# Kernel optimization log

Hardware: AMD Instinct MI355X
Metric: run time of the kernel (lower is better)

## Reference

```python
import jax, jax.numpy as jnp
import numpy as np

N = 100000
E = 640000
D = 128


def _sage_conv(x, src, dst, Wp, bp, Wl, bl, Wr):
    # project=True: project + relu source features before aggregation
    h = jax.nn.relu(x @ Wp.T + bp)            # [N, D]
    msgs = h[src]                              # [E, D] gather
    summed = jax.ops.segment_sum(msgs, dst, num_segments=N)   # [N, D]
    cnt = jax.ops.segment_sum(jnp.ones((msgs.shape[0],), x.dtype), dst, num_segments=N)
    mean = summed / jnp.maximum(cnt, 1.0)[:, None]
    # lin_l on aggregated neighbors (with bias) + lin_r on root (no bias)
    return mean @ Wl.T + bl + x @ Wr.T


def setup_inputs() -> dict:
    key = jax.random.key(0)
    ks = jax.random.split(key, 16)
    s = 1.0 / np.sqrt(D)
    x = jax.random.normal(ks[0], (N, D), dtype=jnp.float32)
    edge_index = jax.random.randint(ks[1], (2, E), 0, N, dtype=jnp.int64)
    params = {}
    for i, base in enumerate(["conv0", "conv1"]):
        params[base + "_Wp"] = jax.random.uniform(ks[2 + 5 * i], (D, D), jnp.float32, -s, s)
        params[base + "_bp"] = jax.random.uniform(ks[3 + 5 * i], (D,), jnp.float32, -s, s)
        params[base + "_Wl"] = jax.random.uniform(ks[4 + 5 * i], (D, D), jnp.float32, -s, s)
        params[base + "_bl"] = jax.random.uniform(ks[5 + 5 * i], (D,), jnp.float32, -s, s)
        params[base + "_Wr"] = jax.random.uniform(ks[6 + 5 * i], (D, D), jnp.float32, -s, s)
    return {"x": x, "edge_index": edge_index, **params}


def reference(x, edge_index,
              conv0_Wp, conv0_bp, conv0_Wl, conv0_bl, conv0_Wr,
              conv1_Wp, conv1_bp, conv1_Wl, conv1_bl, conv1_Wr):
    src, dst = edge_index[0], edge_index[1]
    h = _sage_conv(x, src, dst, conv0_Wp, conv0_bp, conv0_Wl, conv0_bl, conv0_Wr)
    h = jax.nn.relu(h)
    return _sage_conv(h, src, dst, conv1_Wp, conv1_bp, conv1_Wl, conv1_bl, conv1_Wr)
```

## Files before the change

kernel.cpp:

```cpp
#include <hip/hip_runtime.h>

#define DD 128

typedef _Float16 f16;
typedef __attribute__((ext_vector_type(8))) _Float16 v8h;
typedef __attribute__((ext_vector_type(4))) _Float16 v4h;
typedef __attribute__((ext_vector_type(4))) float f32x4;

static inline int cdiv(int a, int b) { return (a + b - 1) / b; }


__global__ __launch_bounds__(256) void zero_kernel(int* __restrict__ p, int n) {
    int i = blockIdx.x * 256 + threadIdx.x;
    if (i < n) p[i] = 0;
}


__global__ __launch_bounds__(256) void count_kernel(const int* __restrict__ dst, int E,
                                                    int* __restrict__ cnt) {
    int e = blockIdx.x * 256 + threadIdx.x;
    if (e < E) atomicAdd(&cnt[dst[e]], 1);
}

__global__ __launch_bounds__(256) void scan1(const int* __restrict__ cnt, int N,
                                             int* __restrict__ bsum) {
    __shared__ int s[256];
    int i = blockIdx.x * 256 + threadIdx.x;
    s[threadIdx.x] = (i < N) ? cnt[i] : 0;
    __syncthreads();
    for (int off = 128; off > 0; off >>= 1) {
        if (threadIdx.x < off) s[threadIdx.x] += s[threadIdx.x + off];
        __syncthreads();
    }
    if (threadIdx.x == 0) bsum[blockIdx.x] = s[0];
}

__global__ __launch_bounds__(512) void scan2(const int* __restrict__ bsum, int NB,
                                             int* __restrict__ boff) {
    __shared__ int s[512];
    int t = threadIdx.x;
    int v = (t < NB) ? bsum[t] : 0;
    s[t] = v;
    __syncthreads();
    for (int off = 1; off < 512; off <<= 1) {
        int x = (t >= off) ? s[t - off] : 0;
        __syncthreads();
        s[t] += x;
        __syncthreads();
    }
    if (t < NB) boff[t] = s[t] - v;
}

__global__ __launch_bounds__(256) void scan3(const int* __restrict__ cnt,
                                             const int* __restrict__ boff, int N,
                                             int* __restrict__ off) {
    __shared__ int s[256];
    int t = threadIdx.x;
    int i = blockIdx.x * 256 + t;
    int v = (i < N) ? cnt[i] : 0;
    s[t] = v;
    __syncthreads();
    for (int o = 1; o < 256; o <<= 1) {
        int x = (t >= o) ? s[t - o] : 0;
        __syncthreads();
        s[t] += x;
        __syncthreads();
    }
    int excl = s[t] - v + boff[blockIdx.x];
    if (i < N) off[i] = excl;
    if (i == N - 1) off[N] = excl + v;
}

__global__ __launch_bounds__(256) void fill_kernel(const int* __restrict__ src,
                                                   const int* __restrict__ dst, int E,
                                                   const int* __restrict__ off,
                                                   int* __restrict__ cnt,
                                                   int* __restrict__ csr) {
    int e = blockIdx.x * 256 + threadIdx.x;
    if (e < E) {
        int d = dst[e];
        int p = atomicSub(&cnt[d], 1) - 1;
        csr[off[d] + p] = src[e];
    }
}


__global__ __launch_bounds__(256) void cvt_w_kernel(const float* __restrict__ W0,
                                                    const float* __restrict__ W1,
                                                    const float* __restrict__ W2,
                                                    const float* __restrict__ W3,
                                                    const float* __restrict__ W4,
                                                    const float* __restrict__ W5,
                                                    f16* __restrict__ out) {
    int mat = blockIdx.x >> 4;
    const float* W = mat == 0 ? W0 : mat == 1 ? W1 : mat == 2 ? W2
                   : mat == 3 ? W3 : mat == 4 ? W4 : W5;
    int base = (blockIdx.x & 15) * 1024 + threadIdx.x * 4;
    float4 v = *(const float4*)(W + base);
    v4h o;
    o[0] = (f16)v.x; o[1] = (f16)v.y; o[2] = (f16)v.z; o[3] = (f16)v.w;
    *(v4h*)(out + mat * 16384 + base) = o;
}


__device__ inline void stage_w(const f16* __restrict__ Wg, f16* __restrict__ smem, int t) {
#pragma unroll
    for (int i = 0; i < 8; ++i) {
        int idx16 = i * 256 + t;
        int col = idx16 >> 4, c16 = idx16 & 15;
        int sc = c16 ^ (col & 7);
        uint4 v = *(const uint4*)(Wg + idx16 * 8);
        *(uint4*)(smem + col * DD + sc * 8) = v;
    }
}

__device__ inline v8h read_b(const f16* __restrict__ smem, int ct, int ki, int l) {
    int col = ct * 16 + (l & 15);
    int c16 = ki * 4 + (l >> 4);
    int sc = c16 ^ (col & 7);
    return *(const v8h*)(smem + col * DD + sc * 8);
}

__device__ inline v8h load_frag16(const f16* __restrict__ A, int row, int kb, int M) {
    if (row >= M) {
        v8h z = {};
        return z;
    }
    return *(const v8h*)(A + (size_t)row * DD + kb);
}


template <typename TA, bool WX>
__global__ __launch_bounds__(256) void mgemm(const TA* __restrict__ A,
                                             const f16* __restrict__ W1,
                                             const float* __restrict__ bias,
                                             f16* __restrict__ OUT,
                                             f16* __restrict__ A16, int M) {
    __shared__ f16 WS[DD * DD];
    int t = threadIdx.x, l = t & 63, w = t >> 6;
    int row0 = blockIdx.x * 128 + w * 32;
    int r = l & 15, cg = l >> 4;

    stage_w(W1, WS, t);

    v8h af[2][4];
#pragma unroll
    for (int rt = 0; rt < 2; ++rt) {
        int row = row0 + rt * 16 + r;
#pragma unroll
        for (int ki = 0; ki < 4; ++ki) {
            int kb = ki * 32 + cg * 8;
            if constexpr (sizeof(TA) == 2) {
                af[rt][ki] = load_frag16(A, row, kb, M);
            } else {
                if (row < M) {
                    float4 a = *(const float4*)(A + (size_t)row * DD + kb);
                    float4 b = *(const float4*)(A + (size_t)row * DD + kb + 4);
                    v8h rr;
                    rr[0] = (f16)a.x; rr[1] = (f16)a.y; rr[2] = (f16)a.z; rr[3] = (f16)a.w;
                    rr[4] = (f16)b.x; rr[5] = (f16)b.y; rr[6] = (f16)b.z; rr[7] = (f16)b.w;
                    af[rt][ki] = rr;
                } else {
                    v8h z = {};
                    af[rt][ki] = z;
                }
            }
            if constexpr (WX) {
                if (row < M) *(v8h*)(A16 + (size_t)row * DD + kb) = af[rt][ki];
            }
        }
    }
    __syncthreads();

    f32x4 acc[2][8];
#pragma unroll
    for (int ct = 0; ct < 8; ++ct) {
        float bv = bias[ct * 16 + r];
        f32x4 b4 = {bv, bv, bv, bv};
        acc[0][ct] = b4;
        acc[1][ct] = b4;
    }

#pragma unroll
    for (int ct = 0; ct < 8; ++ct)
#pragma unroll
        for (int ki = 0; ki < 4; ++ki) {
            v8h b = read_b(WS, ct, ki, l);
            acc[0][ct] = __builtin_amdgcn_mfma_f32_16x16x32_f16(af[0][ki], b, acc[0][ct], 0, 0, 0);
            acc[1][ct] = __builtin_amdgcn_mfma_f32_16x16x32_f16(af[1][ki], b, acc[1][ct], 0, 0, 0);
        }

#pragma unroll
    for (int rt = 0; rt < 2; ++rt)
#pragma unroll
        for (int ct = 0; ct < 8; ++ct)
#pragma unroll
            for (int j = 0; j < 4; ++j) {
                int row = row0 + rt * 16 + cg * 4 + j;
                if (row < M)
                    OUT[(size_t)row * DD + ct * 16 + r] = (f16)fmaxf(acc[rt][ct][j], 0.f);
            }
}


template <typename TO, bool RELU>
__global__ __launch_bounds__(256) void agg_mgemm(const f16* __restrict__ H,
                                                 const int* __restrict__ off,
                                                 const int* __restrict__ csr,
                                                 const f16* __restrict__ Wl,
                                                 const float* __restrict__ bias,
                                                 const f16* __restrict__ Xr,
                                                 const f16* __restrict__ Wr,
                                                 TO* __restrict__ OUT, int M) {
    __shared__ f16 WS[2 * DD * DD];
    int t = threadIdx.x, l = t & 63, w = t >> 6;
    int row0 = blockIdx.x * 128 + w * 32;
    int r = l & 15, cg = l >> 4;

    stage_w(Wl, WS, t);
    stage_w(Wr, WS + DD * DD, t);

    v8h af2[2][4];
#pragma unroll
    for (int rt = 0; rt < 2; ++rt)
#pragma unroll
        for (int ki = 0; ki < 4; ++ki)
            af2[rt][ki] = load_frag16(Xr, row0 + rt * 16 + r, ki * 32 + cg * 8, M);

    float ag[2][4][8];
#pragma unroll
    for (int rt = 0; rt < 2; ++rt)
#pragma unroll
        for (int ki = 0; ki < 4; ++ki)
#pragma unroll
            for (int j = 0; j < 8; ++j) ag[rt][ki][j] = 0.f;

    float inv[2] = {0.f, 0.f};
#pragma unroll
    for (int rt = 0; rt < 2; ++rt) {
        int row = row0 + rt * 16 + r;
        if (row < M) {
            int s = off[row], e = off[row + 1];
            for (int i = s; i < e; ++i) {
                int idx = csr[i];
                const f16* hp = H + (size_t)idx * DD + cg * 8;
#pragma unroll
                for (int ki = 0; ki < 4; ++ki) {
                    v8h v = *(const v8h*)(hp + ki * 32);
#pragma unroll
                    for (int j = 0; j < 8; ++j) ag[rt][ki][j] += (float)v[j];
                }
            }
            int deg = e - s;
            inv[rt] = 1.0f / (float)(deg > 0 ? deg : 1);
        }
    }

    v8h paf[2][4];
#pragma unroll
    for (int rt = 0; rt < 2; ++rt)
#pragma unroll
        for (int ki = 0; ki < 4; ++ki) {
            v8h p;
#pragma unroll
            for (int j = 0; j < 8; ++j) p[j] = (f16)(ag[rt][ki][j] * inv[rt]);
            paf[rt][ki] = p;
        }

    __syncthreads();

    f32x4 acc[2][8];
#pragma unroll
    for (int ct = 0; ct < 8; ++ct) {
        float bv = bias[ct * 16 + r];
        f32x4 b4 = {bv, bv, bv, bv};
        acc[0][ct] = b4;
        acc[1][ct] = b4;
    }

#pragma unroll
    for (int ct = 0; ct < 8; ++ct)
#pragma unroll
        for (int ki = 0; ki < 4; ++ki) {
            v8h b1 = read_b(WS, ct, ki, l);
            acc[0][ct] = __builtin_amdgcn_mfma_f32_16x16x32_f16(paf[0][ki], b1, acc[0][ct], 0, 0, 0);
            acc[1][ct] = __builtin_amdgcn_mfma_f32_16x16x32_f16(paf[1][ki], b1, acc[1][ct], 0, 0, 0);
            v8h b2 = read_b(WS + DD * DD, ct, ki, l);
            acc[0][ct] = __builtin_amdgcn_mfma_f32_16x16x32_f16(af2[0][ki], b2, acc[0][ct], 0, 0, 0);
            acc[1][ct] = __builtin_amdgcn_mfma_f32_16x16x32_f16(af2[1][ki], b2, acc[1][ct], 0, 0, 0);
        }

#pragma unroll
    for (int rt = 0; rt < 2; ++rt)
#pragma unroll
        for (int ct = 0; ct < 8; ++ct)
#pragma unroll
            for (int j = 0; j < 4; ++j) {
                int row = row0 + rt * 16 + cg * 4 + j;
                if (row < M) {
                    float v = acc[rt][ct][j];
                    if (RELU) v = fmaxf(v, 0.f);
                    OUT[(size_t)row * DD + ct * 16 + r] = (TO)v;
                }
            }
}


extern "C" void kernel_launch(void* const* d_in, const int* in_sizes, int n_in,
                              void* d_out, int out_size, void* d_ws, size_t ws_size,
                              hipStream_t stream) {
    const float* x = (const float*)d_in[0];
    const int* ei = (const int*)d_in[1];
    const float* Wp0 = (const float*)d_in[2];
    const float* bp0 = (const float*)d_in[3];
    const float* Wl0 = (const float*)d_in[4];
    const float* bl0 = (const float*)d_in[5];
    const float* Wr0 = (const float*)d_in[6];
    const float* Wp1 = (const float*)d_in[7];
    const float* bp1 = (const float*)d_in[8];
    const float* Wl1 = (const float*)d_in[9];
    const float* bl1 = (const float*)d_in[10];
    const float* Wr1 = (const float*)d_in[11];

    int N = in_sizes[0] / DD;
    int E = in_sizes[1] / 2;
    const int* src = ei;
    const int* dst = ei + E;

    char* ws = (char*)d_ws;
    size_t o = 0;
    auto alloc = [&](size_t bytes) {
        size_t r = o;
        o = (o + bytes + 255) & ~(size_t)255;
        return r;
    };
    f16* w16 = (f16*)(ws + alloc((size_t)6 * DD * DD * 2));
    int* cnt = (int*)(ws + alloc((size_t)N * 4));
    int* off = (int*)(ws + alloc((size_t)(N + 1) * 4));
    int NB = cdiv(N, 256);
    int* bsum = (int*)(ws + alloc((size_t)NB * 4));
    int* boff = (int*)(ws + alloc((size_t)NB * 4));
    int* csr = (int*)(ws + alloc((size_t)E * 4));
    f16* y1 = (f16*)(ws + alloc((size_t)N * DD * 2));
    f16* h2 = (f16*)(ws + alloc((size_t)N * DD * 2));
    f16* h = (f16*)d_out;
    f16* x16 = (f16*)((char*)d_out + (size_t)N * DD * 2);
    (void)ws_size;

    zero_kernel<<<NB, 256, 0, stream>>>(cnt, N);
    count_kernel<<<cdiv(E, 256), 256, 0, stream>>>(dst, E, cnt);
    scan1<<<NB, 256, 0, stream>>>(cnt, N, bsum);
    scan2<<<1, 512, 0, stream>>>(bsum, NB, boff);
    scan3<<<NB, 256, 0, stream>>>(cnt, boff, N, off);
    fill_kernel<<<cdiv(E, 256), 256, 0, stream>>>(src, dst, E, off, cnt, csr);

    cvt_w_kernel<<<96, 256, 0, stream>>>(Wp0, Wl0, Wr0, Wp1, Wl1, Wr1, w16);
    const f16* wp0 = w16 + 0 * 16384;
    const f16* wl0 = w16 + 1 * 16384;
    const f16* wr0 = w16 + 2 * 16384;
    const f16* wp1 = w16 + 3 * 16384;
    const f16* wl1 = w16 + 4 * 16384;
    const f16* wr1 = w16 + 5 * 16384;

    int GB = cdiv(N, 128);
    mgemm<float, true><<<GB, 256, 0, stream>>>(x, wp0, bp0, h, x16, N);
    agg_mgemm<f16, true>
        <<<GB, 256, 0, stream>>>(h, off, csr, wl0, bl0, x16, wr0, y1, N);
    mgemm<f16, false><<<GB, 256, 0, stream>>>(y1, wp1, bp1, h2, nullptr, N);
    agg_mgemm<float, false>
        <<<GB, 256, 0, stream>>>(h2, off, csr, wl1, bl1, y1, wr1, (float*)d_out, N);
}
```

Measured before the change: 250.7 us.

## Split neighbor aggregation into separate wave-per-node gather kernel before dual GEMM

Moves the mean-aggregation gather out of the fused GEMM kernel into a standalone kernel. The standalone kernel assigns one wave per node, splits edges across four lane groups, prefetches two edges ahead, and reduces with shuffles. The GEMM kernel becomes a plain dual GEMM that reads the precomputed mean. This targets the latency-bound serial per-row gather loop inside the GEMM, which had little parallelism. The cost is an extra round trip of an N×D fp16 mean buffer through memory in each layer, plus two extra launches.

```diff
diff --git a/kernel.cpp b/kernel.cpp
--- a/kernel.cpp
+++ b/kernel.cpp
@@ -103,6 +103,48 @@
 }
 
 
+__global__ __launch_bounds__(256) void aggregate_kernel(const f16* __restrict__ h,
+                                                        const int* __restrict__ off,
+                                                        const int* __restrict__ csr,
+                                                        f16* __restrict__ mean, int N) {
+    int n = blockIdx.x * 4 + (threadIdx.x >> 6);
+    int l = threadIdx.x & 63;
+    int g = l >> 4, c = l & 15;
+    if (n >= N) return;
+    int s = off[n], e = off[n + 1];
+    float acc[8] = {0.f, 0.f, 0.f, 0.f, 0.f, 0.f, 0.f, 0.f};
+    int i0 = s + g;
+    int i1 = i0 + 4;
+    v8h v0 = {}, v1 = {};
+    if (i0 < e) v0 = *(const v8h*)(h + (size_t)csr[i0] * DD + c * 8);
+    if (i1 < e) v1 = *(const v8h*)(h + (size_t)csr[i1] * DD + c * 8);
+    while (i0 < e) {
+        int i2 = i1 + 4;
+        v8h v2 = {};
+        if (i2 < e) v2 = *(const v8h*)(h + (size_t)csr[i2] * DD + c * 8);
+#pragma unroll
+        for (int j = 0; j < 8; ++j) acc[j] += (float)v0[j];
+        v0 = v1;
+        v1 = v2;
+        i0 = i1;
+        i1 = i2;
+    }
+#pragma unroll
+    for (int j = 0; j < 8; ++j) {
+        acc[j] += __shfl_xor(acc[j], 16);
+        acc[j] += __shfl_xor(acc[j], 32);
+    }
+    int deg = e - s;
+    float inv = 1.0f / (float)(deg > 0 ? deg : 1);
+    if (g == 0) {
+        v8h o;
+#pragma unroll
+        for (int j = 0; j < 8; ++j) o[j] = (f16)(acc[j] * inv);
+        *(v8h*)(mean + (size_t)n * DD + c * 8) = o;
+    }
+}
+
+
 __device__ inline void stage_w(const f16* __restrict__ Wg, f16* __restrict__ smem, int t) {
 #pragma unroll
     for (int i = 0; i < 8; ++i) {
@@ -131,11 +173,11 @@
 
 
 template <typename TA, bool WX>
-__global__ __launch_bounds__(256) void mgemm(const TA* __restrict__ A,
-                                             const f16* __restrict__ W1,
-                                             const float* __restrict__ bias,
-                                             f16* __restrict__ OUT,
-                                             f16* __restrict__ A16, int M) {
+__global__ __launch_bounds__(256) void proj_gemm(const TA* __restrict__ A,
+                                                 const f16* __restrict__ W1,
+                                                 const float* __restrict__ bias,
+                                                 f16* __restrict__ OUT,
+                                                 f16* __restrict__ A16, int M) {
     __shared__ f16 WS[DD * DD];
     int t = threadIdx.x, l = t & 63, w = t >> 6;
     int row0 = blockIdx.x * 128 + w * 32;
@@ -204,12 +246,10 @@
 
 
 template <typename TO, bool RELU>
-__global__ __launch_bounds__(256) void agg_mgemm(const f16* __restrict__ H,
-                                                 const int* __restrict__ off,
-                                                 const int* __restrict__ csr,
+__global__ __launch_bounds__(256) void dual_gemm(const f16* __restrict__ A,
                                                  const f16* __restrict__ Wl,
                                                  const float* __restrict__ bias,
-                                                 const f16* __restrict__ Xr,
+                                                 const f16* __restrict__ B,
                                                  const f16* __restrict__ Wr,
                                                  TO* __restrict__ OUT, int M) {
     __shared__ f16 WS[2 * DD * DD];
@@ -220,53 +260,15 @@
     stage_w(Wl, WS, t);
     stage_w(Wr, WS + DD * DD, t);
 
-    v8h af2[2][4];
+    v8h afA[2][4], afB[2][4];
 #pragma unroll
     for (int rt = 0; rt < 2; ++rt)
 #pragma unroll
-        for (int ki = 0; ki < 4; ++ki)
-            af2[rt][ki] = load_frag16(Xr, row0 + rt * 16 + r, ki * 32 + cg * 8, M);
-
-    float ag[2][4][8];
-#pragma unroll
-    for (int rt = 0; rt < 2; ++rt)
-#pragma unroll
-        for (int ki = 0; ki < 4; ++ki)
-#pragma unroll
-            for (int j = 0; j < 8; ++j) ag[rt][ki][j] = 0.f;
-
-    float inv[2] = {0.f, 0.f};
-#pragma unroll
-    for (int rt = 0; rt < 2; ++rt) {
-        int row = row0 + rt * 16 + r;
-        if (row < M) {
-            int s = off[row], e = off[row + 1];
-            for (int i = s; i < e; ++i) {
-                int idx = csr[i];
-                const f16* hp = H + (size_t)idx * DD + cg * 8;
-#pragma unroll
-                for (int ki = 0; ki < 4; ++ki) {
-                    v8h v = *(const v8h*)(hp + ki * 32);
-#pragma unroll
-                    for (int j = 0; j < 8; ++j) ag[rt][ki][j] += (float)v[j];
-                }
-            }
-            int deg = e - s;
-            inv[rt] = 1.0f / (float)(deg > 0 ? deg : 1);
+        for (int ki = 0; ki < 4; ++ki) {
+            int row = row0 + rt * 16 + r, kb = ki * 32 + cg * 8;
+            afA[rt][ki] = load_frag16(A, row, kb, M);
+            afB[rt][ki] = load_frag16(B, row, kb, M);
         }
-    }
-
-    v8h paf[2][4];
-#pragma unroll
-    for (int rt = 0; rt < 2; ++rt)
-#pragma unroll
-        for (int ki = 0; ki < 4; ++ki) {
-            v8h p;
-#pragma unroll
-            for (int j = 0; j < 8; ++j) p[j] = (f16)(ag[rt][ki][j] * inv[rt]);
-            paf[rt][ki] = p;
-        }
-
     __syncthreads();
 
     f32x4 acc[2][8];
@@ -283,11 +285,11 @@
 #pragma unroll
         for (int ki = 0; ki < 4; ++ki) {
             v8h b1 = read_b(WS, ct, ki, l);
-            acc[0][ct] = __builtin_amdgcn_mfma_f32_16x16x32_f16(paf[0][ki], b1, acc[0][ct], 0, 0, 0);
-            acc[1][ct] = __builtin_amdgcn_mfma_f32_16x16x32_f16(paf[1][ki], b1, acc[1][ct], 0, 0, 0);
+            acc[0][ct] = __builtin_amdgcn_mfma_f32_16x16x32_f16(afA[0][ki], b1, acc[0][ct], 0, 0, 0);
+            acc[1][ct] = __builtin_amdgcn_mfma_f32_16x16x32_f16(afA[1][ki], b1, acc[1][ct], 0, 0, 0);
             v8h b2 = read_b(WS + DD * DD, ct, ki, l);
-            acc[0][ct] = __builtin_amdgcn_mfma_f32_16x16x32_f16(af2[0][ki], b2, acc[0][ct], 0, 0, 0);
-            acc[1][ct] = __builtin_amdgcn_mfma_f32_16x16x32_f16(af2[1][ki], b2, acc[1][ct], 0, 0, 0);
+            acc[0][ct] = __builtin_amdgcn_mfma_f32_16x16x32_f16(afB[0][ki], b2, acc[0][ct], 0, 0, 0);
+            acc[1][ct] = __builtin_amdgcn_mfma_f32_16x16x32_f16(afB[1][ki], b2, acc[1][ct], 0, 0, 0);
         }
 
 #pragma unroll
@@ -341,8 +343,8 @@
     int* bsum = (int*)(ws + alloc((size_t)NB * 4));
     int* boff = (int*)(ws + alloc((size_t)NB * 4));
     int* csr = (int*)(ws + alloc((size_t)E * 4));
+    f16* mean = (f16*)(ws + alloc((size_t)N * DD * 2));
     f16* y1 = (f16*)(ws + alloc((size_t)N * DD * 2));
-    f16* h2 = (f16*)(ws + alloc((size_t)N * DD * 2));
     f16* h = (f16*)d_out;
     f16* x16 = (f16*)((char*)d_out + (size_t)N * DD * 2);
     (void)ws_size;
@@ -363,10 +365,10 @@
     const f16* wr1 = w16 + 5 * 16384;
 
     int GB = cdiv(N, 128);
-    mgemm<float, true><<<GB, 256, 0, stream>>>(x, wp0, bp0, h, x16, N);
-    agg_mgemm<f16, true>
-        <<<GB, 256, 0, stream>>>(h, off, csr, wl0, bl0, x16, wr0, y1, N);
-    mgemm<f16, false><<<GB, 256, 0, stream>>>(y1, wp1, bp1, h2, nullptr, N);
-    agg_mgemm<float, false>
-        <<<GB, 256, 0, stream>>>(h2, off, csr, wl1, bl1, y1, wr1, (float*)d_out, N);
-}
+    proj_gemm<float, true><<<GB, 256, 0, stream>>>(x, wp0, bp0, h, x16, N);
+    aggregate_kernel<<<cdiv(N, 4), 256, 0, stream>>>(h, off, csr, mean, N);
+    dual_gemm<f16, true><<<GB, 256, 0, stream>>>(mean, wl0, bl0, x16, wr0, y1, N);
+    proj_gemm<f16, false><<<GB, 256, 0, stream>>>(y1, wp1, bp1, h, nullptr, N);
+    aggregate_kernel<<<cdiv(N, 4), 256, 0, stream>>>(h, off, csr, mean, N);
+    dual_gemm<float, false><<<GB, 256, 0, stream>>>(mean, wl1, bl1, y1, wr1, (float*)d_out, N);
+}
```

New measurement: 242.6 us. 1.03x faster.
